# Kernel optimization log

Hardware: AMD Instinct MI355X
Metric: run time of the kernel (lower is better)

Reference implementation:

```python
import jax, jax.numpy as jnp
import numpy as np

N_IN = 10    # input_dim: x has 2**N_IN features
N_OUT = 10   # output_dim: output has 2**N_OUT features
RANK = 10
BATCH = 512
STD = 0.5


def setup_inputs() -> dict:
    key = jax.random.key(0)
    ks = jax.random.split(key, 5)
    x = jax.random.normal(ks[0], (BATCH, 2 ** N_IN), dtype=jnp.float32)
    # Stacked tensor-train cores; each core is (rank, 2, 2, rank) as in the torch module.
    input_cores = STD * jax.random.normal(ks[1], (N_IN, RANK, 2, 2, RANK), dtype=jnp.float32)
    output_cores = STD * jax.random.normal(ks[2], (N_OUT, RANK, 2, 2, RANK), dtype=jnp.float32)
    # central core is (2,)*(N_IN+N_OUT) in the original; stored here as the
    # equivalent (2**N_IN, 2**N_OUT) matrix (identical math, same memory layout).
    central_core = STD * jax.random.normal(ks[3], (2 ** N_IN, 2 ** N_OUT), dtype=jnp.float32)
    bias = STD * jax.random.normal(ks[4], (1, 2 ** N_OUT), dtype=jnp.float32)
    return {"x": x, "input_cores": input_cores, "output_cores": output_cores,
            "central_core": central_core, "bias": bias}


def reference(x, input_cores, output_cores, central_core, bias):
    # Tensor-wheel contraction with a fixed, precomputed path (replaces the
    # per-call greedy tensornetwork contractor). Exact same sum as the original.
    B = x.shape[0]
    n, r = input_cores.shape[0], input_cores.shape[1]
    m = output_cores.shape[0]

    # --- absorb x into the input-core chain ---
    # State S: (B, l0, C_acc, r_cur, Q_rem) where
    #   l0    = open left bond of input core 0 (closes the ring later)
    #   C_acc = accumulated central-core legs c_1..c_i (dim 2^i, c_1 most significant)
    #   Q_rem = remaining input bits of x (x bit 1 is most significant, matching reshape)
    S = jnp.einsum('bpq,lpcs->blcsq', x.reshape(B, 2, -1), input_cores[0])
    for i in range(1, n):
        _, l, C, rc, Q = S.shape
        S = S.reshape(B, l, C, rc, 2, Q // 2)
        S = jnp.einsum('blcrpq,rpds->blcdsq', S, input_cores[i]).reshape(B, l, 2 * C, r, Q // 2)
    S = S[..., 0]  # (B, l0, 2^n, r_n)

    # --- contract the central core over all input-side legs (dominant GEMM) ---
    U = jnp.einsum('blcr,cd->blrd', S, central_core)  # (B, l0, r_n, 2^m)

    # --- sweep through the output-core chain ---
    # State V: (B, l0, P_acc, r_cur, D_rem); P_acc accumulates free output legs
    # p_1..p_j (p_1 most significant), D_rem holds remaining central output legs.
    V = U.reshape(B, r, 1, r, 2 ** m)
    for j in range(m):
        _, l, P, rc, D = V.shape
        V = V.reshape(B, l, P, rc, 2, D // 2)
        V = jnp.einsum('blxrdq,rpds->blxpsq', V, output_cores[j]).reshape(B, l, 2 * P, r, D // 2)

    # --- close the ring: trace l0 (input core 0 left bond) with rgt_m ---
    out = jnp.einsum('blpl->bp', V[..., 0])  # (B, 2^m)
    return out + bias
```

## Files before the change

### kernel.cpp

```cpp
#include <hip/hip_runtime.h>
#include <cstdint>
#include <cstddef>


typedef __attribute__((ext_vector_type(8))) short short8;
typedef __attribute__((ext_vector_type(4))) float f32x4;

static __device__ __forceinline__ unsigned short f2bf(float f) {
  union { float f; unsigned int u; } v; v.f = f;
  unsigned int r = v.u + 0x7FFFu + ((v.u >> 16) & 1u);
  return (unsigned short)(r >> 16);
}
static __device__ __forceinline__ unsigned int pack2(float a, float b) {
  return (unsigned int)f2bf(a) | ((unsigned int)f2bf(b) << 16);
}

static __device__ __forceinline__ int shuf_in(int stg, int u, int dd) {
  if (stg == 0) return ((u >> 4) << 6) | (dd << 4) | ((u & 3) << 2) | ((u >> 2) & 3);
  if (stg == 1) return ((u >> 2) << 4) | (dd << 2) | (u & 3);
  return (u << 2) | dd;
}
static __device__ __forceinline__ int shuf_out(int stg, int u, int dd) {
  if (stg == 0) return (dd << 6) | ((u & 15) << 2) | (u >> 4);
  if (stg == 1) return ((u >> 4) << 6) | (dd << 4) | ((u & 3) << 2) | ((u >> 2) & 3);
  if (stg == 2) return ((u >> 2) << 4) | (dd << 2) | (u & 3);
  return (u << 2) | dd;
}

static __device__ __forceinline__ void mfma_stage80(
    const unsigned short* stc, const unsigned short* __restrict__ Bf,
    int w, int lane, int c15, int quad, f32x4 acc[4][3]) {
  short8 bfr[3][2];
  #pragma unroll
  for (int nt = 0; nt < 3; ++nt) {
    bfr[nt][0] = *(const short8*)&Bf[(nt * 2 + 0) * 512 + lane * 8];
    bfr[nt][1] = *(const short8*)&Bf[(nt * 2 + 1) * 512 + lane * 8];
  }
  #pragma unroll
  for (int rt = 0; rt < 4; ++rt) {
    const int rowA = w * 64 + rt * 16 + c15;
    const short8 a0 = *(const short8*)((const char*)stc + rowA * 80 + quad * 16);
    const int a1off = (quad == 0) ? rowA * 80 + 64 : 0;
    const short8 a1 = *(const short8*)((const char*)stc + a1off);
    #pragma unroll
    for (int nt = 0; nt < 3; ++nt) {
      f32x4 a = {0.f, 0.f, 0.f, 0.f};
      a = __builtin_amdgcn_mfma_f32_16x16x32_bf16(a0, bfr[nt][0], a, 0, 0, 0);
      a = __builtin_amdgcn_mfma_f32_16x16x32_bf16(a1, bfr[nt][1], a, 0, 0, 0);
      acc[rt][nt] = a;
    }
  }
}

template <int STG, bool INPUT>
static __device__ __forceinline__ void stage_writes80(
    unsigned short* dst, const f32x4 acc[4][3], int w, int quad,
    const int* ddv, const int* sv) {
  #pragma unroll
  for (int rt = 0; rt < 4; ++rt) {
    const int u = w * 16 + rt * 4 + quad;
    #pragma unroll
    for (int nt = 0; nt < 3; ++nt) {
      if (sv[nt] < 10) {
        const int dd = ddv[nt];
        const int row = INPUT ? shuf_in(STG, u, dd) : shuf_out(STG, u, dd);
        uint2 v;
        v.x = pack2(acc[rt][nt][0], acc[rt][nt][1]);
        v.y = pack2(acc[rt][nt][2], acc[rt][nt][3]);
        *(uint2*)((char*)dst + row * 80 + sv[nt] * 8) = v;
      }
    }
  }
}

__global__ __launch_bounds__(256) void k0_prep(
    const float* __restrict__ ic, const float* __restrict__ oc,
    const float* __restrict__ cc, unsigned short* __restrict__ Bt,
    float* __restrict__ c2x, unsigned short* __restrict__ bf1,
    unsigned short* __restrict__ bf3, unsigned short* __restrict__ bf3l) {
  const int t = threadIdx.x;
  const int bx = blockIdx.x;
  if (bx < 1024) {
    const int dly = bx;
    const int D = (dly & 3) * 256 + ((dly >> 2) & 3) * 64 + (dly >> 4);
    const int uC = (t >> 2) * 16 + (t & 3);
    ushort4 pk;
    pk.x = f2bf(cc[(size_t)(uC + 0) * 1024 + D]);
    pk.y = f2bf(cc[(size_t)(uC + 4) * 1024 + D]);
    pk.z = f2bf(cc[(size_t)(uC + 8) * 1024 + D]);
    pk.w = f2bf(cc[(size_t)(uC + 12) * 1024 + D]);
    *(ushort4*)&Bt[(size_t)dly * 1024 + 4 * t] = pk;
  } else if (bx == 1024) {
    for (int idx = t; idx < 1600; idx += 256) {
      int L = idx / 160, rem = idx - L * 160;
      int w = rem / 40, r2 = rem - w * 40;
      int pi = r2 / 10, s = r2 - pi * 10;
      int p1 = pi >> 1, p2 = pi & 1, c1 = w >> 1, c2v = w & 1;
      float a = 0.f;
      for (int r1 = 0; r1 < 10; ++r1)
        a += ic[L * 40 + p1 * 20 + c1 * 10 + r1] *
             ic[400 + r1 * 40 + p2 * 20 + c2v * 10 + s];
      c2x[idx] = a;
    }
  } else if (bx == 1025) {
    for (int idx = t; idx < 12288; idx += 256) {
      int j = idx & 7, lane = (idx >> 3) & 63, kc = (idx >> 9) & 1;
      int g2 = idx >> 10, stg = g2 / 3, nt = g2 - stg * 3;
      int c15 = lane & 15, quad = lane >> 4;
      int n = nt * 16 + c15, dd = n / 12, s = n - dd * 12;
      int k = kc * 32 + quad * 8 + j, c = k >> 2, pi = k & 3;
      float v = 0.f;
      if (k < 40 && s < 10) {
        int p1 = pi >> 1, p2 = pi & 1, d1 = dd >> 1, d2 = dd & 1;
        const float* A = ic + (2 * stg + 2) * 400;
        const float* B = ic + (2 * stg + 3) * 400;
        for (int tt = 0; tt < 10; ++tt)
          v += A[c * 40 + p1 * 20 + d1 * 10 + tt] *
               B[tt * 40 + p2 * 20 + d2 * 10 + s];
      }
      bf1[idx] = f2bf(v);
    }
  } else if (bx == 1026) {
    for (int idx = t; idx < 12288; idx += 256) {
      int j = idx & 7, lane = (idx >> 3) & 63, kc = (idx >> 9) & 1;
      int g2 = idx >> 10, stg = g2 / 3, nt = g2 - stg * 3;
      int c15 = lane & 15, quad = lane >> 4;
      int n = nt * 16 + c15, dd = n / 12, s = n - dd * 12;
      int k = kc * 32 + quad * 8 + j, c = k >> 2, pi = k & 3;
      float v = 0.f;
      if (k < 40 && s < 10) {
        int d1 = pi >> 1, d2 = pi & 1, p1 = dd >> 1, p2 = dd & 1;
        const float* A = oc + (2 * stg) * 400;
        const float* B = oc + (2 * stg + 1) * 400;
        for (int tt = 0; tt < 10; ++tt)
          v += A[c * 40 + p1 * 20 + d1 * 10 + tt] *
               B[tt * 40 + p2 * 20 + d2 * 10 + s];
      }
      bf3[idx] = f2bf(v);
    }
  } else {
    for (int idx = t; idx < 10240; idx += 256) {
      int j = idx & 7, lane = (idx >> 3) & 63, kc = (idx >> 9) & 1, L = idx >> 10;
      int c15 = lane & 15, quad = lane >> 4;
      int k = kc * 32 + quad * 8 + j, c = k >> 2, pi = k & 3;
      float v = 0.f;
      if (k < 40 && c15 < 4) {
        int dd = c15, d1 = pi >> 1, d2 = pi & 1, p1 = dd >> 1, p2 = dd & 1;
        for (int tt = 0; tt < 10; ++tt)
          v += oc[8 * 400 + c * 40 + p1 * 20 + d1 * 10 + tt] *
               oc[9 * 400 + tt * 40 + p2 * 20 + d2 * 10 + L];
      }
      bf3l[idx] = f2bf(v);
    }
  }
}

__global__ __launch_bounds__(256, 4) void k1_insweep(
    const float* __restrict__ x, const float* __restrict__ c2x,
    const unsigned short* __restrict__ bf1, unsigned short* __restrict__ S) {
  __shared__ __align__(16) unsigned short st[20480];
  const int t = threadIdx.x, bx = blockIdx.x;
  const int b = bx / 10, L = bx - b * 10;
  const int lane = t & 63, w = t >> 6;
  const int c15 = lane & 15, quad = lane >> 4;
  int ddv[3], sv[3];
  #pragma unroll
  for (int nt = 0; nt < 3; ++nt) {
    int n = nt * 16 + c15; ddv[nt] = n / 12; sv[nt] = n - ddv[nt] * 12;
  }
  unsigned short* bufA = st;
  unsigned short* bufB = st + 10240;
  {
    const float* xb = x + (size_t)b * 1024;
    const float* C2 = c2x + L * 160 + w * 40;
    float accx[4][10];
    #pragma unroll
    for (int g = 0; g < 4; ++g)
      #pragma unroll
      for (int s = 0; s < 10; ++s) accx[g][s] = 0.f;
    #pragma unroll
    for (int pi = 0; pi < 4; ++pi) {
      float xv[4];
      #pragma unroll
      for (int g = 0; g < 4; ++g) xv[g] = xb[pi * 256 + g * 64 + lane];
      #pragma unroll
      for (int s = 0; s < 10; ++s) {
        const float bv = C2[pi * 10 + s];
        #pragma unroll
        for (int g = 0; g < 4; ++g) accx[g][s] = fmaf(xv[g], bv, accx[g][s]);
      }
    }
    const int row = w * 64 + c15 * 4 + quad;
    #pragma unroll
    for (int s = 0; s < 10; ++s) {
      uint2 v;
      v.x = pack2(accx[0][s], accx[1][s]);
      v.y = pack2(accx[2][s], accx[3][s]);
      *(uint2*)((char*)bufA + row * 80 + s * 8) = v;
    }
  }
  __syncthreads();
  f32x4 acc[4][3];
  mfma_stage80(bufA, bf1 + 0 * 3072, w, lane, c15, quad, acc);
  stage_writes80<0, true>(bufB, acc, w, quad, ddv, sv);
  __syncthreads();
  mfma_stage80(bufB, bf1 + 1 * 3072, w, lane, c15, quad, acc);
  stage_writes80<1, true>(bufA, acc, w, quad, ddv, sv);
  __syncthreads();
  mfma_stage80(bufA, bf1 + 2 * 3072, w, lane, c15, quad, acc);
  stage_writes80<2, true>(bufB, acc, w, quad, ddv, sv);
  __syncthreads();
  mfma_stage80(bufB, bf1 + 3 * 3072, w, lane, c15, quad, acc);
  #pragma unroll
  for (int rt = 0; rt < 4; ++rt) {
    const int u = w * 16 + rt * 4 + quad;
    #pragma unroll
    for (int nt = 0; nt < 3; ++nt) {
      if (sv[nt] < 10) {
        uint2 v;
        v.x = pack2(acc[rt][nt][0], acc[rt][nt][1]);
        v.y = pack2(acc[rt][nt][2], acc[rt][nt][3]);
        *(uint2*)&S[((size_t)(bx * 10 + sv[nt])) * 1024 + u * 16 + ddv[nt] * 4] = v;
      }
    }
  }
}

__global__ __launch_bounds__(256) void k2_gemm(
    const unsigned short* __restrict__ A,
    const unsigned short* __restrict__ B,
    unsigned short* __restrict__ U2a,
    unsigned short* __restrict__ U2b) {
  __shared__ __align__(16) unsigned short Atile[2 * 128 * 32];
  __shared__ __align__(16) unsigned short Btile[2 * 128 * 32];
  const int t = threadIdx.x, bx = blockIdx.x;
  const int xcd = bx & 7;
  const int i8 = bx >> 3;
  const int bm = i8 & 7;
  const int bn = (i8 >> 3) * 8 + xcd;
  const int wave = t >> 6, lane = t & 63;
  const int wm = wave & 1, wn = wave >> 1;

  f32x4 acc[4][4];
  #pragma unroll
  for (int i = 0; i < 4; ++i)
    #pragma unroll
    for (int j = 0; j < 4; ++j) acc[i][j] = (f32x4){0.f, 0.f, 0.f, 0.f};

  const int arow = t >> 2, achk = t & 3;
  const unsigned short* Ag = A + (size_t)(bm * 128 + arow) * 1024 + achk * 8;
  const unsigned short* Bg = B + (size_t)(bn * 128 + arow) * 1024 + achk * 8;
  char* ldsA = (char*)Atile + wave * 1024;
  char* ldsB = (char*)Btile + wave * 1024;

  for (int k0 = 0; k0 < 1024; k0 += 64) {
    #pragma unroll
    for (int kk = 0; kk < 2; ++kk) {
      const int ko = k0 + kk * 32;
      __builtin_amdgcn_global_load_lds(
          (const __attribute__((address_space(1))) void*)(Ag + ko),
          (__attribute__((address_space(3))) void*)(ldsA + kk * 8192), 16, 0, 0);
      __builtin_amdgcn_global_load_lds(
          (const __attribute__((address_space(1))) void*)(Ag + 64 * 1024 + ko),
          (__attribute__((address_space(3))) void*)(ldsA + kk * 8192 + 4096), 16, 0, 0);
      __builtin_amdgcn_global_load_lds(
          (const __attribute__((address_space(1))) void*)(Bg + ko),
          (__attribute__((address_space(3))) void*)(ldsB + kk * 8192), 16, 0, 0);
      __builtin_amdgcn_global_load_lds(
          (const __attribute__((address_space(1))) void*)(Bg + 64 * 1024 + ko),
          (__attribute__((address_space(3))) void*)(ldsB + kk * 8192 + 4096), 16, 0, 0);
    }
    __syncthreads();
    const int kq = (lane >> 4) * 8;
    #pragma unroll
    for (int kk = 0; kk < 2; ++kk) {
      short8 af[4], bf[4];
      #pragma unroll
      for (int mt = 0; mt < 4; ++mt)
        af[mt] = *(const short8*)&Atile[kk * 4096 + (wm * 64 + mt * 16 + (lane & 15)) * 32 + kq];
      #pragma unroll
      for (int nt = 0; nt < 4; ++nt)
        bf[nt] = *(const short8*)&Btile[kk * 4096 + (wn * 64 + nt * 16 + (lane & 15)) * 32 + kq];
      #pragma unroll
      for (int mt = 0; mt < 4; ++mt)
        #pragma unroll
        for (int nt = 0; nt < 4; ++nt)
          acc[mt][nt] = __builtin_amdgcn_mfma_f32_16x16x32_bf16(
              af[mt], bf[nt], acc[mt][nt], 0, 0, 0);
    }
    __syncthreads();
  }
  const int quad = lane >> 4;
  const int col0 = bn * 128 + wn * 64 + (lane & 15);
  const int row0 = bm * 128 + wm * 64;
  #pragma unroll
  for (int nt = 0; nt < 4; ++nt) {
    const int n = col0 + nt * 16;
    const int bl = n / 10;
    const int r = n - bl * 10;
    char* dst = (r < 8)
        ? (char*)U2a + (size_t)bl * 16384 + (size_t)r * 8
        : (char*)U2b + (size_t)bl * 4096 + (size_t)(r - 8) * 8;
    const int rb = (r < 8) ? 64 : 16;
    #pragma unroll
    for (int mt = 0; mt < 4; ++mt) {
      const int mp = (row0 + mt * 16 + quad * 4) >> 2;
      uint2 v;
      v.x = pack2(acc[mt][nt][0], acc[mt][nt][1]);
      v.y = pack2(acc[mt][nt][2], acc[mt][nt][3]);
      *(uint2*)(dst + (size_t)mp * rb) = v;
    }
  }
}

__global__ __launch_bounds__(256, 4) void k3_outsweep(
    const unsigned short* __restrict__ U2a, const unsigned short* __restrict__ U2b,
    const unsigned short* __restrict__ bf3, const unsigned short* __restrict__ bf3l,
    const float* __restrict__ bias, float* __restrict__ out) {
  __shared__ __align__(16) unsigned short st[20480];
  const int t = threadIdx.x, bx = blockIdx.x;
  const int b = bx / 10, L = bx - b * 10;
  const int lane = t & 63, w = t >> 6;
  const int c15 = lane & 15, quad = lane >> 4;
  int ddv[3], sv[3];
  #pragma unroll
  for (int nt = 0; nt < 3; ++nt) {
    int n = nt * 16 + c15; ddv[nt] = n / 12; sv[nt] = n - ddv[nt] * 12;
  }
  unsigned short* bufA = st;
  unsigned short* bufB = st + 10240;
  f32x4 acc[4][3];
  {
    short8 bfr[3][2];
    #pragma unroll
    for (int nt = 0; nt < 3; ++nt) {
      bfr[nt][0] = *(const short8*)&bf3[(nt * 2 + 0) * 512 + lane * 8];
      bfr[nt][1] = *(const short8*)&bf3[(nt * 2 + 1) * 512 + lane * 8];
    }
    const char* Ua = (const char*)U2a + (size_t)bx * 16384;
    const char* Ub = (const char*)U2b + (size_t)bx * 4096;
    #pragma unroll
    for (int rt = 0; rt < 4; ++rt) {
      const int m = w * 64 + rt * 16 + c15;
      const short8 a0 = *(const short8*)(Ua + m * 64 + quad * 16);
      const short8 a1 = *(const short8*)(Ub + m * 16);
      #pragma unroll
      for (int nt = 0; nt < 3; ++nt) {
        f32x4 a = {0.f, 0.f, 0.f, 0.f};
        a = __builtin_amdgcn_mfma_f32_16x16x32_bf16(a0, bfr[nt][0], a, 0, 0, 0);
        a = __builtin_amdgcn_mfma_f32_16x16x32_bf16(a1, bfr[nt][1], a, 0, 0, 0);
        acc[rt][nt] = a;
      }
    }
    stage_writes80<0, false>(bufA, acc, w, quad, ddv, sv);
  }
  __syncthreads();
  mfma_stage80(bufA, bf3 + 1 * 3072, w, lane, c15, quad, acc);
  stage_writes80<1, false>(bufB, acc, w, quad, ddv, sv);
  __syncthreads();
  mfma_stage80(bufB, bf3 + 2 * 3072, w, lane, c15, quad, acc);
  stage_writes80<2, false>(bufA, acc, w, quad, ddv, sv);
  __syncthreads();
  mfma_stage80(bufA, bf3 + 3 * 3072, w, lane, c15, quad, acc);
  stage_writes80<3, false>(bufB, acc, w, quad, ddv, sv);
  __syncthreads();
  {
    const unsigned short* Bf = bf3l + L * 1024;
    const short8 b0 = *(const short8*)&Bf[lane * 8];
    const short8 b1 = *(const short8*)&Bf[512 + lane * 8];
    #pragma unroll
    for (int rt = 0; rt < 4; ++rt) {
      const int rowA = w * 64 + rt * 16 + c15;
      const short8 a0 = *(const short8*)((const char*)bufB + rowA * 80 + quad * 16);
      const int a1off = (quad == 0) ? rowA * 80 + 64 : 0;
      const short8 a1 = *(const short8*)((const char*)bufB + a1off);
      f32x4 a = {0.f, 0.f, 0.f, 0.f};
      a = __builtin_amdgcn_mfma_f32_16x16x32_bf16(a0, b0, a, 0, 0, 0);
      a = __builtin_amdgcn_mfma_f32_16x16x32_bf16(a1, b1, a, 0, 0, 0);
      if (c15 < 4) {
        const int u = w * 16 + rt * 4 + quad;
        #pragma unroll
        for (int i = 0; i < 4; ++i) {
          const int oidx = u * 16 + i * 4 + c15;
          float v = a[i];
          if (L == 0) v += bias[oidx];
          atomicAdd(&out[(size_t)b * 1024 + oidx], v);
        }
      }
    }
  }
}

extern "C" void kernel_launch(void* const* d_in, const int* in_sizes, int n_in,
                              void* d_out, int out_size, void* d_ws, size_t ws_size,
                              hipStream_t stream) {
  (void)in_sizes; (void)n_in; (void)ws_size;
  const float* x    = (const float*)d_in[0];
  const float* ic   = (const float*)d_in[1];
  const float* oc   = (const float*)d_in[2];
  const float* cc   = (const float*)d_in[3];
  const float* bias = (const float*)d_in[4];
  float* out = (float*)d_out;

  char* ws = (char*)d_ws;
  unsigned short* S    = (unsigned short*)(ws);
  unsigned short* U2a  = (unsigned short*)(ws + 104857600);
  unsigned short* U2b  = (unsigned short*)(ws + 188743680);
  unsigned short* Bt   = (unsigned short*)(ws + 209715200);
  float*          c2x  = (float*)(ws + 211812352);
  unsigned short* bf1  = (unsigned short*)(ws + 211818752);
  unsigned short* bf3  = (unsigned short*)(ws + 211843328);
  unsigned short* bf3l = (unsigned short*)(ws + 211867904);

  hipMemsetAsync(d_out, 0, (size_t)out_size * sizeof(float), stream);
  k0_prep<<<1028, 256, 0, stream>>>(ic, oc, cc, Bt, c2x, bf1, bf3, bf3l);
  k1_insweep<<<5120, 256, 0, stream>>>(x, c2x, bf1, S);
  k2_gemm<<<3200, 256, 0, stream>>>(Bt, S, U2a, U2b);
  k3_outsweep<<<5120, 256, 0, stream>>>(U2a, U2b, bf3, bf3l, bias, out);
}
```

Before: 362.4 us.

## Rewrite central GEMM with 256x256 tiles, double-buffered LDS and swizzled loads

The central-core GEMM now uses 512-thread blocks with 256x256 output tiles and 800 blocks instead of 3200. Global-to-LDS loads are double-buffered across k-steps with explicit vmcnt waits and barriers, so the next stage loads while the current one runs on MFMA. An XOR swizzle on the LDS layout is meant to avoid bank conflicts, and s_setprio is raised around the MFMA bursts. The larger tiles improve operand reuse and cut global traffic. In exchange they use 128KB of LDS and many accumulator registers per block, which lowers occupancy, and the hand-written waitcnt sequencing is fragile.

```diff
diff --git a/kernel.cpp b/kernel.cpp
--- a/kernel.cpp
+++ b/kernel.cpp
@@ -226,89 +226,118 @@
   }
 }
 
-__global__ __launch_bounds__(256) void k2_gemm(
+
+#define K2_STAGE(T, KS)                                                        \
+  {                                                                            \
+    const unsigned short* gs = gptr + (T) * 64 + (KS) * 32;                    \
+    char* lb = lds_stage + (((T) & 1) << 16) + ((KS) << 15);                   \
+    _Pragma("unroll")                                                          \
+    for (int i = 0; i < 4; ++i)                                                \
+      __builtin_amdgcn_global_load_lds(                                        \
+          (const __attribute__((address_space(1))) void*)(gs + (i << 14)),     \
+          (__attribute__((address_space(3))) void*)(lb + (i << 10)), 16, 0, 0);\
+  }
+
+#define K2_PHASE(T, KS, DO_STAGE, VMCNT_ASM, DO_SYNC)                          \
+  {                                                                            \
+    const char* rb = ldsb + (((T) & 1) << 16) + ((KS) << 15);                  \
+    short8 afr[8], bfr[4];                                                     \
+    _Pragma("unroll")                                                          \
+    for (int mt = 0; mt < 8; ++mt)                                             \
+      afr[mt] = *(const short8*)(rb + ((arow0 + (mt << 4)) << 6) + aswz);      \
+    _Pragma("unroll")                                                          \
+    for (int nt = 0; nt < 4; ++nt)                                             \
+      bfr[nt] = *(const short8*)(rb + 16384 + ((brow0 + (nt << 4)) << 6) + aswz);\
+    __builtin_amdgcn_s_setprio(1);                                             \
+    _Pragma("unroll")                                                          \
+    for (int mt = 0; mt < 8; ++mt)                                             \
+      _Pragma("unroll")                                                        \
+      for (int nt = 0; nt < 4; ++nt)                                           \
+        acc[mt][nt] = __builtin_amdgcn_mfma_f32_16x16x32_bf16(                 \
+            afr[mt], bfr[nt], acc[mt][nt], 0, 0, 0);                           \
+    __builtin_amdgcn_s_setprio(0);                                             \
+    if (DO_SYNC) {                                                             \
+      asm volatile("s_waitcnt lgkmcnt(0)" ::: "memory");                       \
+      __builtin_amdgcn_sched_barrier(0);                                       \
+      __builtin_amdgcn_s_barrier();         \
+      __builtin_amdgcn_sched_barrier(0);                                       \
+      if (DO_STAGE) K2_STAGE((T) + 2, (KS))                                    \
+      __builtin_amdgcn_sched_barrier(0);                                       \
+      VMCNT_ASM;                             \
+      __builtin_amdgcn_s_barrier();              \
+      __builtin_amdgcn_sched_barrier(0);                                       \
+    }                                                                          \
+  }
+
+__global__ __launch_bounds__(512, 2) void k2_gemm(
     const unsigned short* __restrict__ A,
     const unsigned short* __restrict__ B,
     unsigned short* __restrict__ U2a,
     unsigned short* __restrict__ U2b) {
-  __shared__ __align__(16) unsigned short Atile[2 * 128 * 32];
-  __shared__ __align__(16) unsigned short Btile[2 * 128 * 32];
-  const int t = threadIdx.x, bx = blockIdx.x;
-  const int xcd = bx & 7;
-  const int i8 = bx >> 3;
-  const int bm = i8 & 7;
-  const int bn = (i8 >> 3) * 8 + xcd;
-  const int wave = t >> 6, lane = t & 63;
-  const int wm = wave & 1, wn = wave >> 1;
-
-  f32x4 acc[4][4];
-  #pragma unroll
-  for (int i = 0; i < 4; ++i)
+  __shared__ __align__(16) char ldsb[131072];
+  const int tid = threadIdx.x, bx = blockIdx.x;
+  const int bid = (bx & 7) * 100 + (bx >> 3);
+  const int bm = bid & 3, bn = bid >> 2;
+  const int Mtile0 = bm << 8, Ntile0 = bn << 8;
+  const int w = tid >> 6, lane = tid & 63;
+  const int c15 = lane & 15, quad = lane >> 4;
+  const int wm = w >> 2, wn = w & 3;
+
+  const int arow0 = (wm << 7) + c15;
+  const int brow0 = (wn << 6) + c15;
+  const int aswz = ((quad ^ ((c15 >> 1) & 3)) << 4);
+
+  const int sec = w >> 2;
+  const int rsub = ((w & 3) << 6) + (lane >> 2);
+  const unsigned short* gbase =
+      (sec == 0) ? (A + ((size_t)(Mtile0 + rsub) << 10))
+                 : (B + ((size_t)(Ntile0 + rsub) << 10));
+  const unsigned short* gptr = gbase + (((lane & 3) ^ ((lane >> 3) & 3)) << 3);
+  char* lds_stage = ldsb + (sec << 14) + ((w & 3) << 12);
+
+  f32x4 acc[8][4];
+  #pragma unroll
+  for (int i = 0; i < 8; ++i)
     #pragma unroll
     for (int j = 0; j < 4; ++j) acc[i][j] = (f32x4){0.f, 0.f, 0.f, 0.f};
 
-  const int arow = t >> 2, achk = t & 3;
-  const unsigned short* Ag = A + (size_t)(bm * 128 + arow) * 1024 + achk * 8;
-  const unsigned short* Bg = B + (size_t)(bn * 128 + arow) * 1024 + achk * 8;
-  char* ldsA = (char*)Atile + wave * 1024;
-  char* ldsB = (char*)Btile + wave * 1024;
-
-  for (int k0 = 0; k0 < 1024; k0 += 64) {
-    #pragma unroll
-    for (int kk = 0; kk < 2; ++kk) {
-      const int ko = k0 + kk * 32;
-      __builtin_amdgcn_global_load_lds(
-          (const __attribute__((address_space(1))) void*)(Ag + ko),
-          (__attribute__((address_space(3))) void*)(ldsA + kk * 8192), 16, 0, 0);
-      __builtin_amdgcn_global_load_lds(
-          (const __attribute__((address_space(1))) void*)(Ag + 64 * 1024 + ko),
-          (__attribute__((address_space(3))) void*)(ldsA + kk * 8192 + 4096), 16, 0, 0);
-      __builtin_amdgcn_global_load_lds(
-          (const __attribute__((address_space(1))) void*)(Bg + ko),
-          (__attribute__((address_space(3))) void*)(ldsB + kk * 8192), 16, 0, 0);
-      __builtin_amdgcn_global_load_lds(
-          (const __attribute__((address_space(1))) void*)(Bg + 64 * 1024 + ko),
-          (__attribute__((address_space(3))) void*)(ldsB + kk * 8192 + 4096), 16, 0, 0);
-    }
-    __syncthreads();
-    const int kq = (lane >> 4) * 8;
-    #pragma unroll
-    for (int kk = 0; kk < 2; ++kk) {
-      short8 af[4], bf[4];
-      #pragma unroll
-      for (int mt = 0; mt < 4; ++mt)
-        af[mt] = *(const short8*)&Atile[kk * 4096 + (wm * 64 + mt * 16 + (lane & 15)) * 32 + kq];
-      #pragma unroll
-      for (int nt = 0; nt < 4; ++nt)
-        bf[nt] = *(const short8*)&Btile[kk * 4096 + (wn * 64 + nt * 16 + (lane & 15)) * 32 + kq];
-      #pragma unroll
-      for (int mt = 0; mt < 4; ++mt)
-        #pragma unroll
-        for (int nt = 0; nt < 4; ++nt)
-          acc[mt][nt] = __builtin_amdgcn_mfma_f32_16x16x32_bf16(
-              af[mt], bf[nt], acc[mt][nt], 0, 0, 0);
-    }
-    __syncthreads();
-  }
-  const int quad = lane >> 4;
-  const int col0 = bn * 128 + wn * 64 + (lane & 15);
-  const int row0 = bm * 128 + wm * 64;
+  K2_STAGE(0, 0)
+  K2_STAGE(0, 1)
+  K2_STAGE(1, 0)
+  K2_STAGE(1, 1)
+  asm volatile("s_waitcnt vmcnt(12)" ::: "memory");
+  __builtin_amdgcn_s_barrier();
+  __builtin_amdgcn_sched_barrier(0);
+
+  #define K2_VM12 asm volatile("s_waitcnt vmcnt(12)" ::: "memory")
+  #pragma unroll 2
+  for (int kt = 0; kt < 14; ++kt) {
+    K2_PHASE(kt, 0, true, K2_VM12, true)
+    K2_PHASE(kt, 1, true, K2_VM12, true)
+  }
+  K2_PHASE(14, 0, false, asm volatile("s_waitcnt vmcnt(8)" ::: "memory"), true)
+  K2_PHASE(14, 1, false, asm volatile("s_waitcnt vmcnt(4)" ::: "memory"), true)
+  K2_PHASE(15, 0, false, asm volatile("s_waitcnt vmcnt(0)" ::: "memory"), true)
+  K2_PHASE(15, 1, false, (void)0, false)
+
+  const int col0 = Ntile0 + (wn << 6) + c15;
+  const int rowb = Mtile0 + (wm << 7);
   #pragma unroll
   for (int nt = 0; nt < 4; ++nt) {
-    const int n = col0 + nt * 16;
+    const int n = col0 + (nt << 4);
     const int bl = n / 10;
     const int r = n - bl * 10;
     char* dst = (r < 8)
         ? (char*)U2a + (size_t)bl * 16384 + (size_t)r * 8
         : (char*)U2b + (size_t)bl * 4096 + (size_t)(r - 8) * 8;
-    const int rb = (r < 8) ? 64 : 16;
-    #pragma unroll
-    for (int mt = 0; mt < 4; ++mt) {
-      const int mp = (row0 + mt * 16 + quad * 4) >> 2;
+    const int rbs = (r < 8) ? 64 : 16;
+    #pragma unroll
+    for (int mt = 0; mt < 8; ++mt) {
+      const int mp = (rowb + (mt << 4) + (quad << 2)) >> 2;
       uint2 v;
       v.x = pack2(acc[mt][nt][0], acc[mt][nt][1]);
       v.y = pack2(acc[mt][nt][2], acc[mt][nt][3]);
-      *(uint2*)(dst + (size_t)mp * rb) = v;
+      *(uint2*)(dst + (size_t)mp * rbs) = v;
     }
   }
 }
@@ -415,6 +444,6 @@
   hipMemsetAsync(d_out, 0, (size_t)out_size * sizeof(float), stream);
   k0_prep<<<1028, 256, 0, stream>>>(ic, oc, cc, Bt, c2x, bf1, bf3, bf3l);
   k1_insweep<<<5120, 256, 0, stream>>>(x, c2x, bf1, S);
-  k2_gemm<<<3200, 256, 0, stream>>>(Bt, S, U2a, U2b);
+  k2_gemm<<<800, 512, 0, stream>>>(Bt, S, U2a, U2b);
   k3_outsweep<<<5120, 256, 0, stream>>>(U2a, U2b, bf3, bf3l, bias, out);
 }
```

Result: no change. 362.3 us (-0.0%).
